# Kernel tuning notes

Measured on AMD Instinct MI355X. Metric: run time of the kernel, lower is better.

The kernel has to match this reference:

```python
import jax, jax.numpy as jnp
import numpy as np

B, IN, HS = 4096, 1024, 1024


def setup_inputs() -> dict:
    key = jax.random.key(0)
    ks = jax.random.split(key, 20)
    inp = {
        "x": jax.random.normal(ks[0], (B, IN), jnp.float32),
        "h": jax.random.normal(ks[1], (B, HS), jnp.float32),
        "c": jax.random.normal(ks[2], (B, HS), jnp.float32),
    }
    names_x = ["Wix", "Wfx", "Wgx", "Wox"]
    names_h = ["Wih", "Wfh", "Wgh", "Woh"]
    bnames_x = ["bix", "bfx", "bgx", "box"]
    bnames_h = ["bih", "bfh", "bgh", "boh"]
    k = 3
    for wn, bn in zip(names_x, bnames_x):
        inp[wn] = jax.random.normal(ks[k], (HS, IN), jnp.float32) * 0.02; k += 1
        inp[bn] = jax.random.normal(ks[k], (HS,), jnp.float32) * 0.02; k += 1
    for wn, bn in zip(names_h, bnames_h):
        inp[wn] = jax.random.normal(ks[k], (HS, HS), jnp.float32) * 0.02; k += 1
        inp[bn] = jax.random.normal(ks[k], (HS,), jnp.float32) * 0.02; k += 1
    return inp


def reference(x, h, c,
              Wix, bix, Wfx, bfx, Wgx, bgx, Wox, box,
              Wih, bih, Wfh, bfh, Wgh, bgh, Woh, boh):
    # torch Linear: y = x @ W.T + b
    i = jax.nn.sigmoid(x @ Wix.T + bix + h @ Wih.T + bih)
    f = jax.nn.sigmoid(x @ Wfx.T + bfx + h @ Wfh.T + bfh)
    g = jnp.tanh(x @ Wgx.T + bgx + h @ Wgh.T + bgh)
    o = jax.nn.sigmoid(x @ Wox.T + box + h @ Woh.T + boh)
    c_new = f * c + i * g
    h_new = o * jnp.tanh(c_new)
    return (h_new, c_new)
```

## Files before the change

kernel.cpp:

```cpp
#include <hip/hip_runtime.h>
#include <hip/hip_bf16.h>
#include <stdint.h>

#define BATCH  4096
#define IN_DIM 1024
#define HS     1024
#define K_DIM  2048
#define N_DIM  4096
#define BK 64
#define NKT (K_DIM / BK)
#define HALF_BYTES 16384
#define TPB_BYTES  (NKT * HALF_BYTES)

typedef __bf16 bf16x8 __attribute__((ext_vector_type(8)));
typedef float  f32x4  __attribute__((ext_vector_type(4)));

__device__ __forceinline__ unsigned short f2bf(float f) {
    union { float f; uint32_t u; } a; a.f = f;
    uint32_t r = a.u + 0x7FFF + ((a.u >> 16) & 1);
    return (unsigned short)(r >> 16);
}
__device__ __forceinline__ uint32_t pk2(float a, float b) {
    return (uint32_t)f2bf(a) | ((uint32_t)f2bf(b) << 16);
}

__device__ __forceinline__ void load16_lds(const void* g, void* l) {
    __builtin_amdgcn_global_load_lds(
        (const __attribute__((address_space(1))) uint32_t*)g,
        (__attribute__((address_space(3))) uint32_t*)(uintptr_t)l,
        16, 0, 0);
}
__device__ __forceinline__ void stage16k(const char* g, char* l, int wid, int lane) {
    load16_lds(g + wid * 1024 + lane * 16,        l + wid * 1024);
    load16_lds(g + 8192 + wid * 1024 + lane * 16, l + 8192 + wid * 1024);
}

__device__ __forceinline__ float sigf(float x)  { return 1.0f / (1.0f + __expf(-x)); }
__device__ __forceinline__ float tanhf_(float x){ return 1.0f - 2.0f / (__expf(2.0f * x) + 1.0f); }

#define BAR()   __builtin_amdgcn_s_barrier()
#define PRIO(x) __builtin_amdgcn_s_setprio(x)

__device__ __forceinline__ void rdA4(bf16x8 (&d)[4], const char* base, int kb0, int kb1) {
    d[0] = *(const bf16x8*)(base + kb0);
    d[1] = *(const bf16x8*)(base + kb1);
    d[2] = *(const bf16x8*)(base + 2048 + kb0);
    d[3] = *(const bf16x8*)(base + 2048 + kb1);
}
__device__ __forceinline__ void rdB8(bf16x8 (&d)[8], const char* base, int kb0, int kb1) {
    #pragma unroll
    for (int j = 0; j < 4; ++j) {
        d[j]     = *(const bf16x8*)(base + j * 2048 + kb0);
        d[4 + j] = *(const bf16x8*)(base + j * 2048 + kb1);
    }
}
template<int Q>
__device__ __forceinline__ void mfq(f32x4 (&acc)[8][4], const bf16x8 (&a)[4],
                                    const bf16x8 (&b)[8]) {
    #pragma unroll
    for (int mf = 0; mf < 2; ++mf)
        #pragma unroll
        for (int ks = 0; ks < 2; ++ks)
            #pragma unroll
            for (int j = 0; j < 4; ++j)
                acc[2 * Q + mf][j] = __builtin_amdgcn_mfma_f32_16x16x32_bf16(
                    a[mf * 2 + ks], b[ks * 4 + j], acc[2 * Q + mf][j], 0, 0, 0);
}

__global__ void pack_kernel(const float* __restrict__ x, const float* __restrict__ h,
                            const float* __restrict__ Wix, const float* __restrict__ Wfx,
                            const float* __restrict__ Wgx, const float* __restrict__ Wox,
                            const float* __restrict__ Wih, const float* __restrict__ Wfh,
                            const float* __restrict__ Wgh, const float* __restrict__ Woh,
                            uint4* __restrict__ Apk, uint4* __restrict__ Bpk)
{
    int t = blockIdx.x * blockDim.x + threadIdx.x;
    const int NCHUNK = (BATCH * K_DIM) / 8;
    bool isB = t >= NCHUNK;
    int ci = isB ? (t - NCHUNK) : t;

    int cb  = ci & 7;
    int row = (ci >> 3) & 127;
    int kt  = (ci >> 10) & 31;
    int bt  = ci >> 15;

    int k0 = kt * BK + ((cb ^ (row & 7)) << 3);
    int gr = bt * 128 + row;

    const float* src;
    if (!isB) {
        src = (k0 < IN_DIM) ? (x + (size_t)gr * IN_DIM + k0)
                            : (h + (size_t)gr * HS + (k0 - IN_DIM));
    } else {
        int q = (gr >> 4) & 3;
        int u = ((gr >> 6) << 4) | (gr & 15);
        const float* Wq = (k0 < IN_DIM)
            ? ((q == 0) ? Wix : (q == 1) ? Wfx : (q == 2) ? Wgx : Wox)
            : ((q == 0) ? Wih : (q == 1) ? Wfh : (q == 2) ? Wgh : Woh);
        int kk = (k0 < IN_DIM) ? k0 : (k0 - IN_DIM);
        src = Wq + (size_t)u * 1024 + kk;
    }
    float4 v0 = ((const float4*)src)[0];
    float4 v1 = ((const float4*)src)[1];
    uint4 o;
    o.x = pk2(v0.x, v0.y); o.y = pk2(v0.z, v0.w);
    o.z = pk2(v1.x, v1.y); o.w = pk2(v1.z, v1.w);
    (isB ? Bpk : Apk)[ci] = o;
}

__global__ void __launch_bounds__(512, 2)
gemm_kernel(const char* __restrict__ Apk, const char* __restrict__ Bpk,
            const float* __restrict__ c,
            const float* __restrict__ bix, const float* __restrict__ bfx,
            const float* __restrict__ bgx, const float* __restrict__ box_,
            const float* __restrict__ bih, const float* __restrict__ bfh,
            const float* __restrict__ bgh, const float* __restrict__ boh,
            float* __restrict__ out)
{
    __shared__ uint4 lds4[131072 / 16];
    char* lds = (char*)lds4;

    const int tid  = threadIdx.x;
    const int lane = tid & 63;
    const int wid  = tid >> 6;
    const int wm   = wid >> 2;
    const int wn   = wid & 3;
    const int fr   = lane & 15;
    const int kg   = lane >> 4;

    const int phys = blockIdx.x;
    const int virt = (phys & 7) * 32 + (phys >> 3);
    const int bn   = virt & 15;
    const int bm   = virt >> 4;

    const char* gA = Apk + (size_t)(bm * 2) * TPB_BYTES;
    const char* gB = Bpk + (size_t)(bn * 2) * TPB_BYTES;

    const int kb0   = (kg * 16) ^ ((fr & 7) << 4);
    const int kb1   = kb0 ^ 64;
    const int aBase = wm * 16384 + fr * 128;
    const int bBase = 32768 + wn * 8192 + fr * 128;

    f32x4 acc[8][4] = {};
    bf16x8 aE[4], aO[4], bA_[8], bB_[8];

    stage16k(gA + (size_t)(0 * NKT + 0) * HALF_BYTES, lds + 0,     wid, lane);
    stage16k(gA + (size_t)(1 * NKT + 0) * HALF_BYTES, lds + 16384, wid, lane);
    stage16k(gB + (size_t)(0 * NKT + 0) * HALF_BYTES, lds + 32768, wid, lane);
    stage16k(gB + (size_t)(1 * NKT + 0) * HALF_BYTES, lds + 49152, wid, lane);
    stage16k(gB + (size_t)(0 * NKT + 1) * HALF_BYTES, lds + 65536 + 32768, wid, lane);
    stage16k(gB + (size_t)(1 * NKT + 1) * HALF_BYTES, lds + 65536 + 49152, wid, lane);
    stage16k(gA + (size_t)(0 * NKT + 1) * HALF_BYTES, lds + 65536 + 0,     wid, lane);
    stage16k(gA + (size_t)(1 * NKT + 1) * HALF_BYTES, lds + 65536 + 16384, wid, lane);
    asm volatile("s_waitcnt vmcnt(8)" ::: "memory");
    BAR();
    rdB8(bA_, lds + bBase, kb0, kb1);
    rdA4(aE, lds + aBase, kb0, kb1);

#define TILE(L, LN, KT2, BCUR, BNXT)                                          \
    {                                                                 \
      asm volatile("s_waitcnt vmcnt(4)" ::: "memory");                        \
      stage16k(gB + (size_t)(0 * NKT + (KT2)) * HALF_BYTES, (L) + 32768, wid, lane); \
      rdA4(aO, (L) + aBase + 4096, kb0, kb1);                                 \
      rdB8(BNXT, (LN) + bBase, kb0, kb1);                                     \
      PRIO(1); mfq<0>(acc, aE, BCUR); PRIO(0); BAR();                         \
                                                                      \
      stage16k(gB + (size_t)(1 * NKT + (KT2)) * HALF_BYTES, (L) + 49152, wid, lane); \
      rdA4(aE, (L) + aBase + 8192, kb0, kb1);                                 \
      PRIO(1); mfq<1>(acc, aO, BCUR); PRIO(0); BAR();                         \
                                                                      \
      stage16k(gA + (size_t)(0 * NKT + (KT2)) * HALF_BYTES, (L) + 0, wid, lane); \
      rdA4(aO, (L) + aBase + 12288, kb0, kb1);                                \
      PRIO(1); mfq<2>(acc, aE, BCUR); PRIO(0); BAR();                         \
                                                                      \
      asm volatile("s_waitcnt vmcnt(6)" ::: "memory");                        \
      stage16k(gA + (size_t)(1 * NKT + (KT2)) * HALF_BYTES, (L) + 16384, wid, lane); \
      rdA4(aE, (LN) + aBase, kb0, kb1);                                       \
      PRIO(1); mfq<3>(acc, aO, BCUR); PRIO(0); BAR();                         \
    }

    for (int it = 0; it < NKT / 2; ++it) {
        const int k2e = (it * 2 + 2) & (NKT - 1);
        const int k2o = (it * 2 + 3) & (NKT - 1);
        TILE(lds,         lds + 65536, k2e, bA_, bB_);
        TILE(lds + 65536, lds,         k2o, bB_, bA_);
    }
#undef TILE

    const int u  = bn * 64 + wn * 16 + fr;
    const int r0 = bm * 256 + wm * 128;
    const float bi = bix[u] + bih[u];
    const float bf = bfx[u] + bfh[u];
    const float bg = bgx[u] + bgh[u];
    const float bo = box_[u] + boh[u];
    float* hout = out;
    float* cout = out + (size_t)BATCH * HS;

    #pragma unroll
    for (int ai = 0; ai < 8; ++ai) {
        const int rowb = r0 + ai * 16 + kg * 4;
        #pragma unroll
        for (int r = 0; r < 4; ++r) {
            const size_t idx = (size_t)(rowb + r) * HS + u;
            float iv = sigf  (acc[ai][0][r] + bi);
            float fv = sigf  (acc[ai][1][r] + bf);
            float gv = tanhf_(acc[ai][2][r] + bg);
            float ov = sigf  (acc[ai][3][r] + bo);
            float cn = fv * c[idx] + iv * gv;
            hout[idx] = ov * tanhf_(cn);
            cout[idx] = cn;
        }
    }
}

extern "C" void kernel_launch(void* const* d_in, const int* in_sizes, int n_in,
                              void* d_out, int out_size, void* d_ws, size_t ws_size,
                              hipStream_t stream)
{
    const float* x   = (const float*)d_in[0];
    const float* h   = (const float*)d_in[1];
    const float* c   = (const float*)d_in[2];
    const float* Wix = (const float*)d_in[3];  const float* bix = (const float*)d_in[4];
    const float* Wfx = (const float*)d_in[5];  const float* bfx = (const float*)d_in[6];
    const float* Wgx = (const float*)d_in[7];  const float* bgx = (const float*)d_in[8];
    const float* Wox = (const float*)d_in[9];  const float* box_ = (const float*)d_in[10];
    const float* Wih = (const float*)d_in[11]; const float* bih = (const float*)d_in[12];
    const float* Wfh = (const float*)d_in[13]; const float* bfh = (const float*)d_in[14];
    const float* Wgh = (const float*)d_in[15]; const float* bgh = (const float*)d_in[16];
    const float* Woh = (const float*)d_in[17]; const float* boh = (const float*)d_in[18];

    char* ws = (char*)d_ws;
    uint4* Apk = (uint4*)ws;
    uint4* Bpk = (uint4*)(ws + (size_t)16 * 1024 * 1024);

    pack_kernel<<<8192, 256, 0, stream>>>(x, h, Wix, Wfx, Wgx, Wox,
                                          Wih, Wfh, Wgh, Woh, Apk, Bpk);
    gemm_kernel<<<256, 512, 0, stream>>>((const char*)Apk, (const char*)Bpk, c,
                                         bix, bfx, bgx, box_, bih, bfh, bgh, boh,
                                         (float*)d_out);
}
```

Before: 83.51 us.

## Restructure GEMM main loop into eight-phase schedule with single A register buffer

Rewrites the double-buffered LDS pipeline so each half-iteration reads one A quarter into a single register set and issues global-to-LDS stages at different points, with barriers on both sides of each MFMA group. The prologue stages fewer tiles, and the A tile for the next step is loaded just in time. The goal is to cut register pressure and rebalance load and compute overlap. In exchange it doubles the barrier count and removes A prefetch across phases, which can expose LDS latency.

```diff
diff --git a/kernel.cpp b/kernel.cpp
--- a/kernel.cpp
+++ b/kernel.cpp
@@ -40,6 +40,7 @@
 
 #define BAR()   __builtin_amdgcn_s_barrier()
 #define PRIO(x) __builtin_amdgcn_s_setprio(x)
+#define VMC(n)  asm volatile("s_waitcnt vmcnt(" #n ")" ::: "memory")
 
 __device__ __forceinline__ void rdA4(bf16x8 (&d)[4], const char* base, int kb0, int kb1) {
     d[0] = *(const bf16x8*)(base + kb0);
@@ -119,6 +120,8 @@
 {
     __shared__ uint4 lds4[131072 / 16];
     char* lds = (char*)lds4;
+    char* L0  = lds;
+    char* L1  = lds + 65536;
 
     const int tid  = threadIdx.x;
     const int lane = tid & 63;
@@ -138,54 +141,64 @@
 
     const int kb0   = (kg * 16) ^ ((fr & 7) << 4);
     const int kb1   = kb0 ^ 64;
-    const int aBase = wm * 16384 + fr * 128;
-    const int bBase = 32768 + wn * 8192 + fr * 128;
+    const int aOff  = wm * 16384 + fr * 128;
+    const int bOff  = 32768 + wn * 8192 + fr * 128;
 
     f32x4 acc[8][4] = {};
-    bf16x8 aE[4], aO[4], bA_[8], bB_[8];
-
-    stage16k(gA + (size_t)(0 * NKT + 0) * HALF_BYTES, lds + 0,     wid, lane);
-    stage16k(gA + (size_t)(1 * NKT + 0) * HALF_BYTES, lds + 16384, wid, lane);
-    stage16k(gB + (size_t)(0 * NKT + 0) * HALF_BYTES, lds + 32768, wid, lane);
-    stage16k(gB + (size_t)(1 * NKT + 0) * HALF_BYTES, lds + 49152, wid, lane);
-    stage16k(gB + (size_t)(0 * NKT + 1) * HALF_BYTES, lds + 65536 + 32768, wid, lane);
-    stage16k(gB + (size_t)(1 * NKT + 1) * HALF_BYTES, lds + 65536 + 49152, wid, lane);
-    stage16k(gA + (size_t)(0 * NKT + 1) * HALF_BYTES, lds + 65536 + 0,     wid, lane);
-    stage16k(gA + (size_t)(1 * NKT + 1) * HALF_BYTES, lds + 65536 + 16384, wid, lane);
-    asm volatile("s_waitcnt vmcnt(8)" ::: "memory");
+    bf16x8 aQ[4], bCur[8], bNxt[8];
+
+    stage16k(gA + (size_t)(0 * NKT + 0) * HALF_BYTES, L0 + 0,     wid, lane);
+    stage16k(gA + (size_t)(1 * NKT + 0) * HALF_BYTES, L0 + 16384, wid, lane);
+    stage16k(gB + (size_t)(0 * NKT + 0) * HALF_BYTES, L0 + 32768, wid, lane);
+    stage16k(gB + (size_t)(1 * NKT + 0) * HALF_BYTES, L0 + 49152, wid, lane);
+    stage16k(gB + (size_t)(0 * NKT + 1) * HALF_BYTES, L1 + 32768, wid, lane);
+    stage16k(gB + (size_t)(1 * NKT + 1) * HALF_BYTES, L1 + 49152, wid, lane);
+    VMC(4);
     BAR();
-    rdB8(bA_, lds + bBase, kb0, kb1);
-    rdA4(aE, lds + aBase, kb0, kb1);
-
-#define TILE(L, LN, KT2, BCUR, BNXT)                                          \
-    {                                                                 \
-      asm volatile("s_waitcnt vmcnt(4)" ::: "memory");                        \
-      stage16k(gB + (size_t)(0 * NKT + (KT2)) * HALF_BYTES, (L) + 32768, wid, lane); \
-      rdA4(aO, (L) + aBase + 4096, kb0, kb1);                                 \
-      rdB8(BNXT, (LN) + bBase, kb0, kb1);                                     \
-      PRIO(1); mfq<0>(acc, aE, BCUR); PRIO(0); BAR();                         \
-                                                                      \
-      stage16k(gB + (size_t)(1 * NKT + (KT2)) * HALF_BYTES, (L) + 49152, wid, lane); \
-      rdA4(aE, (L) + aBase + 8192, kb0, kb1);                                 \
-      PRIO(1); mfq<1>(acc, aO, BCUR); PRIO(0); BAR();                         \
-                                                                      \
-      stage16k(gA + (size_t)(0 * NKT + (KT2)) * HALF_BYTES, (L) + 0, wid, lane); \
-      rdA4(aO, (L) + aBase + 12288, kb0, kb1);                                \
-      PRIO(1); mfq<2>(acc, aE, BCUR); PRIO(0); BAR();                         \
-                                                                      \
-      asm volatile("s_waitcnt vmcnt(6)" ::: "memory");                        \
-      stage16k(gA + (size_t)(1 * NKT + (KT2)) * HALF_BYTES, (L) + 16384, wid, lane); \
-      rdA4(aE, (LN) + aBase, kb0, kb1);                                       \
-      PRIO(1); mfq<3>(acc, aO, BCUR); PRIO(0); BAR();                         \
-    }
+    rdB8(bCur, L0 + bOff, kb0, kb1);
 
     for (int it = 0; it < NKT / 2; ++it) {
-        const int k2e = (it * 2 + 2) & (NKT - 1);
-        const int k2o = (it * 2 + 3) & (NKT - 1);
-        TILE(lds,         lds + 65536, k2e, bA_, bB_);
-        TILE(lds + 65536, lds,         k2o, bB_, bA_);
-    }
-#undef TILE
+        const int t  = it * 2;
+        const int w1 = t + 1;
+        const int w2 = (t + 2) & (NKT - 1);
+        const int w3 = (t + 3) & (NKT - 1);
+
+        rdA4(aQ, L0 + aOff, kb0, kb1);
+        stage16k(gA + (size_t)(0 * NKT + w1) * HALF_BYTES, L1 + 0,     wid, lane);
+        stage16k(gA + (size_t)(1 * NKT + w1) * HALF_BYTES, L1 + 16384, wid, lane);
+        BAR(); PRIO(1); mfq<0>(acc, aQ, bCur); PRIO(0); BAR();
+
+        rdA4(aQ, L0 + aOff + 4096, kb0, kb1);
+        BAR(); PRIO(1); mfq<1>(acc, aQ, bCur); PRIO(0); BAR();
+
+        rdA4(aQ, L0 + aOff + 8192, kb0, kb1);
+        stage16k(gB + (size_t)(0 * NKT + w2) * HALF_BYTES, L0 + 32768, wid, lane);
+        VMC(2);
+        BAR(); PRIO(1); mfq<2>(acc, aQ, bCur); PRIO(0); BAR();
+
+        rdA4(aQ, L0 + aOff + 12288, kb0, kb1);
+        rdB8(bNxt, L1 + bOff, kb0, kb1);
+        stage16k(gB + (size_t)(1 * NKT + w2) * HALF_BYTES, L0 + 49152, wid, lane);
+        BAR(); PRIO(1); mfq<3>(acc, aQ, bCur); PRIO(0); BAR();
+
+        rdA4(aQ, L1 + aOff, kb0, kb1);
+        stage16k(gA + (size_t)(0 * NKT + w2) * HALF_BYTES, L0 + 0,     wid, lane);
+        stage16k(gA + (size_t)(1 * NKT + w2) * HALF_BYTES, L0 + 16384, wid, lane);
+        BAR(); PRIO(1); mfq<0>(acc, aQ, bNxt); PRIO(0); BAR();
+
+        rdA4(aQ, L1 + aOff + 4096, kb0, kb1);
+        BAR(); PRIO(1); mfq<1>(acc, aQ, bNxt); PRIO(0); BAR();
+
+        rdA4(aQ, L1 + aOff + 8192, kb0, kb1);
+        stage16k(gB + (size_t)(0 * NKT + w3) * HALF_BYTES, L1 + 32768, wid, lane);
+        VMC(2);
+        BAR(); PRIO(1); mfq<2>(acc, aQ, bNxt); PRIO(0); BAR();
+
+        rdA4(aQ, L1 + aOff + 12288, kb0, kb1);
+        rdB8(bCur, L0 + bOff, kb0, kb1);
+        stage16k(gB + (size_t)(1 * NKT + w3) * HALF_BYTES, L1 + 49152, wid, lane);
+        BAR(); PRIO(1); mfq<3>(acc, aQ, bNxt); PRIO(0); BAR();
+    }
 
     const int u  = bn * 64 + wn * 16 + fr;
     const int r0 = bm * 256 + wm * 128;
```

New measurement: 85.63 us (median of 2 runs). 2.5% more time.

## Replace fine-grained interleaved staging with simple double-buffer pipeline and prefetch c

Applied to the files above, without the earlier changes.

Replaces the hand-tuned per-quarter interleaving of global-to-LDS staging, partial vmcnt waits and per-quarter barriers with a plain double-buffered loop. Each iteration waits for all loads, issues the whole next tile, then computes the current one. It also prefetches the c values before the last tile's MFMAs so their latency overlaps compute. The result is simpler code with fewer barriers, but the full vmcnt(0) wait per tile can expose load latency that the previous schedule hid.

```diff
diff --git a/kernel.cpp b/kernel.cpp
--- a/kernel.cpp
+++ b/kernel.cpp
@@ -40,6 +40,7 @@
 
 #define BAR()   __builtin_amdgcn_s_barrier()
 #define PRIO(x) __builtin_amdgcn_s_setprio(x)
+#define VMC0()  asm volatile("s_waitcnt vmcnt(0)" ::: "memory")
 
 __device__ __forceinline__ void rdA4(bf16x8 (&d)[4], const char* base, int kb0, int kb1) {
     d[0] = *(const bf16x8*)(base + kb0);
@@ -138,77 +139,82 @@
 
     const int kb0   = (kg * 16) ^ ((fr & 7) << 4);
     const int kb1   = kb0 ^ 64;
-    const int aBase = wm * 16384 + fr * 128;
-    const int bBase = 32768 + wn * 8192 + fr * 128;
+    const int aOff  = wm * 16384 + fr * 128;
+    const int bOff  = 32768 + wn * 8192 + fr * 128;
 
     f32x4 acc[8][4] = {};
-    bf16x8 aE[4], aO[4], bA_[8], bB_[8];
+    bf16x8 a0[4], a1[4], a2[4], a3[4], bC[8];
 
     stage16k(gA + (size_t)(0 * NKT + 0) * HALF_BYTES, lds + 0,     wid, lane);
     stage16k(gA + (size_t)(1 * NKT + 0) * HALF_BYTES, lds + 16384, wid, lane);
     stage16k(gB + (size_t)(0 * NKT + 0) * HALF_BYTES, lds + 32768, wid, lane);
     stage16k(gB + (size_t)(1 * NKT + 0) * HALF_BYTES, lds + 49152, wid, lane);
-    stage16k(gB + (size_t)(0 * NKT + 1) * HALF_BYTES, lds + 65536 + 32768, wid, lane);
-    stage16k(gB + (size_t)(1 * NKT + 1) * HALF_BYTES, lds + 65536 + 49152, wid, lane);
-    stage16k(gA + (size_t)(0 * NKT + 1) * HALF_BYTES, lds + 65536 + 0,     wid, lane);
-    stage16k(gA + (size_t)(1 * NKT + 1) * HALF_BYTES, lds + 65536 + 16384, wid, lane);
-    asm volatile("s_waitcnt vmcnt(8)" ::: "memory");
-    BAR();
-    rdB8(bA_, lds + bBase, kb0, kb1);
-    rdA4(aE, lds + aBase, kb0, kb1);
-
-#define TILE(L, LN, KT2, BCUR, BNXT)                                          \
-    {                                                                 \
-      asm volatile("s_waitcnt vmcnt(4)" ::: "memory");                        \
-      stage16k(gB + (size_t)(0 * NKT + (KT2)) * HALF_BYTES, (L) + 32768, wid, lane); \
-      rdA4(aO, (L) + aBase + 4096, kb0, kb1);                                 \
-      rdB8(BNXT, (LN) + bBase, kb0, kb1);                                     \
-      PRIO(1); mfq<0>(acc, aE, BCUR); PRIO(0); BAR();                         \
-                                                                      \
-      stage16k(gB + (size_t)(1 * NKT + (KT2)) * HALF_BYTES, (L) + 49152, wid, lane); \
-      rdA4(aE, (L) + aBase + 8192, kb0, kb1);                                 \
-      PRIO(1); mfq<1>(acc, aO, BCUR); PRIO(0); BAR();                         \
-                                                                      \
-      stage16k(gA + (size_t)(0 * NKT + (KT2)) * HALF_BYTES, (L) + 0, wid, lane); \
-      rdA4(aO, (L) + aBase + 12288, kb0, kb1);                                \
-      PRIO(1); mfq<2>(acc, aE, BCUR); PRIO(0); BAR();                         \
-                                                                      \
-      asm volatile("s_waitcnt vmcnt(6)" ::: "memory");                        \
-      stage16k(gA + (size_t)(1 * NKT + (KT2)) * HALF_BYTES, (L) + 16384, wid, lane); \
-      rdA4(aE, (LN) + aBase, kb0, kb1);                                       \
-      PRIO(1); mfq<3>(acc, aO, BCUR); PRIO(0); BAR();                         \
-    }
-
-    for (int it = 0; it < NKT / 2; ++it) {
-        const int k2e = (it * 2 + 2) & (NKT - 1);
-        const int k2o = (it * 2 + 3) & (NKT - 1);
-        TILE(lds,         lds + 65536, k2e, bA_, bB_);
-        TILE(lds + 65536, lds,         k2o, bB_, bA_);
-    }
-#undef TILE
+
+    for (int t = 0; t < NKT - 1; ++t) {
+        char* L  = lds + (t & 1) * 65536;
+        char* Ln = lds + ((t & 1) ^ 1) * 65536;
+        VMC0();
+        BAR();
+        stage16k(gA + (size_t)(0 * NKT + t + 1) * HALF_BYTES, Ln + 0,     wid, lane);
+        stage16k(gA + (size_t)(1 * NKT + t + 1) * HALF_BYTES, Ln + 16384, wid, lane);
+        stage16k(gB + (size_t)(0 * NKT + t + 1) * HALF_BYTES, Ln + 32768, wid, lane);
+        stage16k(gB + (size_t)(1 * NKT + t + 1) * HALF_BYTES, Ln + 49152, wid, lane);
+        rdB8(bC, L + bOff, kb0, kb1);
+        rdA4(a0, L + aOff,         kb0, kb1);
+        rdA4(a1, L + aOff + 4096,  kb0, kb1);
+        PRIO(1); mfq<0>(acc, a0, bC); PRIO(0);
+        rdA4(a2, L + aOff + 8192,  kb0, kb1);
+        PRIO(1); mfq<1>(acc, a1, bC); PRIO(0);
+        rdA4(a3, L + aOff + 12288, kb0, kb1);
+        PRIO(1); mfq<2>(acc, a2, bC); PRIO(0);
+        PRIO(1); mfq<3>(acc, a3, bC); PRIO(0);
+    }
 
     const int u  = bn * 64 + wn * 16 + fr;
     const int r0 = bm * 256 + wm * 128;
-    const float bi = bix[u] + bih[u];
-    const float bf = bfx[u] + bfh[u];
-    const float bg = bgx[u] + bgh[u];
-    const float bo = box_[u] + boh[u];
-    float* hout = out;
-    float* cout = out + (size_t)BATCH * HS;
-
-    #pragma unroll
-    for (int ai = 0; ai < 8; ++ai) {
-        const int rowb = r0 + ai * 16 + kg * 4;
+    {
+        char* L = lds + ((NKT - 1) & 1) * 65536;
+        VMC0();
+        BAR();
+        float cpre[8][4];
         #pragma unroll
-        for (int r = 0; r < 4; ++r) {
-            const size_t idx = (size_t)(rowb + r) * HS + u;
-            float iv = sigf  (acc[ai][0][r] + bi);
-            float fv = sigf  (acc[ai][1][r] + bf);
-            float gv = tanhf_(acc[ai][2][r] + bg);
-            float ov = sigf  (acc[ai][3][r] + bo);
-            float cn = fv * c[idx] + iv * gv;
-            hout[idx] = ov * tanhf_(cn);
-            cout[idx] = cn;
+        for (int ai = 0; ai < 8; ++ai) {
+            const int rowb = r0 + ai * 16 + kg * 4;
+            #pragma unroll
+            for (int r = 0; r < 4; ++r)
+                cpre[ai][r] = c[(size_t)(rowb + r) * HS + u];
+        }
+        const float bi = bix[u] + bih[u];
+        const float bf = bfx[u] + bfh[u];
+        const float bg = bgx[u] + bgh[u];
+        const float bo = box_[u] + boh[u];
+
+        rdB8(bC, L + bOff, kb0, kb1);
+        rdA4(a0, L + aOff,         kb0, kb1);
+        rdA4(a1, L + aOff + 4096,  kb0, kb1);
+        PRIO(1); mfq<0>(acc, a0, bC); PRIO(0);
+        rdA4(a2, L + aOff + 8192,  kb0, kb1);
+        PRIO(1); mfq<1>(acc, a1, bC); PRIO(0);
+        rdA4(a3, L + aOff + 12288, kb0, kb1);
+        PRIO(1); mfq<2>(acc, a2, bC); PRIO(0);
+        PRIO(1); mfq<3>(acc, a3, bC); PRIO(0);
+
+        float* hout = out;
+        float* cout = out + (size_t)BATCH * HS;
+        #pragma unroll
+        for (int ai = 0; ai < 8; ++ai) {
+            const int rowb = r0 + ai * 16 + kg * 4;
+            #pragma unroll
+            for (int r = 0; r < 4; ++r) {
+                const size_t idx = (size_t)(rowb + r) * HS + u;
+                float iv = sigf  (acc[ai][0][r] + bi);
+                float fv = sigf  (acc[ai][1][r] + bf);
+                float gv = tanhf_(acc[ai][2][r] + bg);
+                float ov = sigf  (acc[ai][3][r] + bo);
+                float cn = fv * cpre[ai][r] + iv * gv;
+                hout[idx] = ov * tanhf_(cn);
+                cout[idx] = cn;
+            }
         }
     }
 }
```

Result: slower. 95.06 us (+13.8%).
